# Optimization experiments

Measured on AMD Instinct MI355X. Metric: run time of the kernel, lower is better.

Reference implementation:

```python
import jax, jax.numpy as jnp
import numpy as np

B, S, T, D = 32, 8, 128, 768   # batch, num_sentences, seq_len, embedding_dim
A, L = 8, 8                    # num_args, arg_length


def _extract(sentence_embeddings, sentence_ids, token_ids):
    """Vectorized form of extract_embeddings_from_ids.

    For each (b, s, a): average, over nonzero token ids l, the embedding at the
    sentence position whose id equals token_ids[b,s,a,l]. token_id == 0 is skipped.
    sentence_ids are unique per sentence, so each id matches exactly one position
    (the only case where the original loop yields shape [B,S,A,D]).
    """
    valid = token_ids != 0                                            # [B,S,A,L]
    # match[b,s,a,l,t] = token matches sentence position t (and token is nonzero)
    match = (token_ids[..., None] == sentence_ids[:, :, None, None, :]) & valid[..., None]
    # gather matched embeddings per token: [B,S,A,L,D]
    gathered = jnp.einsum('bsalt,bstd->bsald', match.astype(sentence_embeddings.dtype),
                          sentence_embeddings)
    n_valid = jnp.maximum(valid.sum(-1), 1).astype(sentence_embeddings.dtype)  # [B,S,A]
    return gathered.sum(axis=3) / n_valid[..., None]                  # [B,S,A,D]


def setup_inputs() -> dict:
    key = jax.random.key(0)
    k_emb, k_p, k_a0, k_a1 = jax.random.split(key, 4)
    sentence_embeddings = jax.random.normal(k_emb, (B, S, T, D), dtype=jnp.float32)
    # unique token ids 1..T per sentence (0 is reserved as padding/skip)
    sentence_ids = jnp.broadcast_to(jnp.arange(1, T + 1, dtype=jnp.int64), (B, S, T))
    predicate_ids = jax.random.randint(k_p, (B, S, A, L), 0, T, dtype=jnp.int64)
    arg0_ids = jax.random.randint(k_a0, (B, S, A, L), 0, T, dtype=jnp.int64)
    arg1_ids = jax.random.randint(k_a1, (B, S, A, L), 0, T, dtype=jnp.int64)
    return {
        'sentence_embeddings': sentence_embeddings,
        'sentence_ids': sentence_ids,
        'predicate_ids': predicate_ids,
        'arg0_ids': arg0_ids,
        'arg1_ids': arg1_ids,
    }


def reference(sentence_embeddings, sentence_ids, predicate_ids, arg0_ids, arg1_ids):
    sentence_average_embeddings = sentence_embeddings.mean(axis=2)     # [B,S,D]
    predicate_embeddings = _extract(sentence_embeddings, sentence_ids, predicate_ids)
    arg0_embeddings = _extract(sentence_embeddings, sentence_ids, arg0_ids)
    arg1_embeddings = _extract(sentence_embeddings, sentence_ids, arg1_ids)
    return (sentence_average_embeddings, predicate_embeddings,
            arg0_embeddings, arg1_embeddings)
```

## Files before the change

### kernel.cpp

```cpp
#include <hip/hip_runtime.h>

namespace {
constexpr int B_ = 32, S_ = 8, T_ = 128, D_ = 768, A_ = 8, L_ = 8;
constexpr int BS = B_ * S_;
constexpr int MEAN_ELEMS = BS * D_;
constexpr int EXT_ELEMS  = BS * A_ * D_;
constexpr int TSPLIT = 4, TCH = T_ / TSPLIT;
constexpr int D4 = D_ / 4;
constexpr int RED_BLOCKS = BS * D4 / 256;
constexpr int EXT_BLOCKS = BS * A_;
constexpr size_t WS_FLOATS = (size_t)TSPLIT * BS * D_;

__global__ void __launch_bounds__(192) k_mean_partial(
    const float* __restrict__ emb, float* __restrict__ ws)
{
    int blk = blockIdx.x;
    int bs = blk >> 2, ch = blk & 3;
    int tid = threadIdx.x;
    const float4* p = reinterpret_cast<const float4*>(emb + (size_t)bs * T_ * D_)
                      + (size_t)(ch * TCH) * D4 + tid;
    float4 acc = {0.f, 0.f, 0.f, 0.f};
    #pragma unroll 8
    for (int t = 0; t < TCH; ++t) {
        float4 v = p[(size_t)t * D4];
        acc.x += v.x; acc.y += v.y; acc.z += v.z; acc.w += v.w;
    }
    reinterpret_cast<float4*>(ws)[(size_t)(ch * BS + bs) * D4 + tid] = acc;
}

__global__ void __launch_bounds__(192) k_mean_full(
    const float* __restrict__ emb, float* __restrict__ out)
{
    int bs = blockIdx.x, tid = threadIdx.x;
    const float4* p = reinterpret_cast<const float4*>(emb + (size_t)bs * T_ * D_) + tid;
    float4 acc = {0.f, 0.f, 0.f, 0.f};
    #pragma unroll 8
    for (int t = 0; t < T_; ++t) {
        float4 v = p[(size_t)t * D4];
        acc.x += v.x; acc.y += v.y; acc.z += v.z; acc.w += v.w;
    }
    const float s = 1.0f / T_;
    float4 r = {acc.x * s, acc.y * s, acc.z * s, acc.w * s};
    reinterpret_cast<float4*>(out)[(size_t)bs * D4 + tid] = r;
}

template <bool WITH_RED>
__global__ void __launch_bounds__(256) k_tail(
    const float* __restrict__ emb,
    const int* __restrict__ sids,
    const int* __restrict__ pred,
    const int* __restrict__ arg0,
    const int* __restrict__ arg1,
    const float* __restrict__ ws,
    float* __restrict__ out)
{
    int blk = blockIdx.x;
    int tid = threadIdx.x;

    if (WITH_RED) {
        if (blk < RED_BLOCKS) {
            int idx = blk * 256 + tid;
            const float4* w = reinterpret_cast<const float4*>(ws);
            float4 a = w[idx];
            float4 b = w[(size_t)BS * D4 + idx];
            float4 c = w[2 * (size_t)BS * D4 + idx];
            float4 d = w[3 * (size_t)BS * D4 + idx];
            const float s = 1.0f / T_;
            float4 r = {(a.x + b.x + c.x + d.x) * s, (a.y + b.y + c.y + d.y) * s,
                        (a.z + b.z + c.z + d.z) * s, (a.w + b.w + c.w + d.w) * s};
            reinterpret_cast<float4*>(out)[idx] = r;
            return;
        }
        blk -= RED_BLOCKS;
    }

    int bs = blk >> 3, a = blk & 7;
    constexpr int NT = 3 * L_;
    __shared__ int toks[NT];
    __shared__ int pos[NT];
    __shared__ float invs[3];

    if (tid < NT) {
        int e = tid >> 3, l = tid & 7;
        const int* p = (e == 0) ? pred : ((e == 1) ? arg0 : arg1);
        toks[tid] = p[(size_t)(bs * A_ + a) * L_ + l];
        pos[tid] = -1;
    }
    __syncthreads();
    if (tid < T_) {
        int id = sids[(size_t)bs * T_ + tid];
        #pragma unroll
        for (int i = 0; i < NT; ++i)
            if (toks[i] != 0 && toks[i] == id) pos[i] = tid;
    } else if (tid >= 128 && tid < 128 + 3) {
        int e = tid - 128, n = 0;
        #pragma unroll
        for (int l = 0; l < L_; ++l) n += (toks[e * L_ + l] != 0);
        invs[e] = 1.0f / (float)(n < 1 ? 1 : n);
    }
    __syncthreads();

    const float* base = emb + (size_t)bs * T_ * D_;
    float acc[3][3] = {};
    #pragma unroll
    for (int e = 0; e < 3; ++e) {
        #pragma unroll
        for (int l = 0; l < L_; ++l) {
            int p = pos[e * L_ + l];
            if (p >= 0) {
                const float* row = base + (size_t)p * D_;
                acc[e][0] += row[tid];
                acc[e][1] += row[tid + 256];
                acc[e][2] += row[tid + 512];
            }
        }
    }
    #pragma unroll
    for (int e = 0; e < 3; ++e) {
        float iv = invs[e];
        float* o = out + MEAN_ELEMS + (size_t)e * EXT_ELEMS + (size_t)(bs * A_ + a) * D_;
        o[tid]       = acc[e][0] * iv;
        o[tid + 256] = acc[e][1] * iv;
        o[tid + 512] = acc[e][2] * iv;
    }
}
}

extern "C" void kernel_launch(void* const* d_in, const int* in_sizes, int n_in,
                              void* d_out, int out_size, void* d_ws, size_t ws_size,
                              hipStream_t stream) {
    const float* emb  = (const float*)d_in[0];
    const int*   sids = (const int*)d_in[1];
    const int*   pred = (const int*)d_in[2];
    const int*   arg0 = (const int*)d_in[3];
    const int*   arg1 = (const int*)d_in[4];
    float* out = (float*)d_out;
    float* ws  = (float*)d_ws;

    if (ws_size >= WS_FLOATS * sizeof(float)) {
        k_mean_partial<<<dim3(BS * TSPLIT), dim3(192), 0, stream>>>(emb, ws);
        k_tail<true><<<dim3(RED_BLOCKS + EXT_BLOCKS), dim3(256), 0, stream>>>(
            emb, sids, pred, arg0, arg1, ws, out);
    } else {
        k_mean_full<<<dim3(BS), dim3(192), 0, stream>>>(emb, out);
        k_tail<false><<<dim3(EXT_BLOCKS), dim3(256), 0, stream>>>(
            emb, sids, pred, arg0, arg1, ws, out);
    }
}
```

Baseline: 45.65 us.

## Fuse sentence-mean and extraction into a single kernel launch

Replaces the two-kernel path (split-T partial mean into a workspace, then a reduce+extract kernel) with one kernel. The first 256 blocks each compute a full 128-row mean directly, and the remaining blocks do the token extraction. This removes one launch and the workspace round trip. In exchange each mean block does a long serial 128-row reduction with only 192 active threads, so the mean blocks may become the critical path.

Measured after the change: 43.85 us. 1.04x faster.

```diff
diff --git a/kernel.cpp b/kernel.cpp
--- a/kernel.cpp
+++ b/kernel.cpp
@@ -5,76 +5,39 @@
 constexpr int BS = B_ * S_;
 constexpr int MEAN_ELEMS = BS * D_;
 constexpr int EXT_ELEMS  = BS * A_ * D_;
-constexpr int TSPLIT = 4, TCH = T_ / TSPLIT;
 constexpr int D4 = D_ / 4;
-constexpr int RED_BLOCKS = BS * D4 / 256;
-constexpr int EXT_BLOCKS = BS * A_;
-constexpr size_t WS_FLOATS = (size_t)TSPLIT * BS * D_;
+constexpr int MEAN_BLOCKS = BS;
+constexpr int EXT_BLOCKS  = BS * A_;
 
-__global__ void __launch_bounds__(192) k_mean_partial(
-    const float* __restrict__ emb, float* __restrict__ ws)
-{
-    int blk = blockIdx.x;
-    int bs = blk >> 2, ch = blk & 3;
-    int tid = threadIdx.x;
-    const float4* p = reinterpret_cast<const float4*>(emb + (size_t)bs * T_ * D_)
-                      + (size_t)(ch * TCH) * D4 + tid;
-    float4 acc = {0.f, 0.f, 0.f, 0.f};
-    #pragma unroll 8
-    for (int t = 0; t < TCH; ++t) {
-        float4 v = p[(size_t)t * D4];
-        acc.x += v.x; acc.y += v.y; acc.z += v.z; acc.w += v.w;
-    }
-    reinterpret_cast<float4*>(ws)[(size_t)(ch * BS + bs) * D4 + tid] = acc;
-}
-
-__global__ void __launch_bounds__(192) k_mean_full(
-    const float* __restrict__ emb, float* __restrict__ out)
-{
-    int bs = blockIdx.x, tid = threadIdx.x;
-    const float4* p = reinterpret_cast<const float4*>(emb + (size_t)bs * T_ * D_) + tid;
-    float4 acc = {0.f, 0.f, 0.f, 0.f};
-    #pragma unroll 8
-    for (int t = 0; t < T_; ++t) {
-        float4 v = p[(size_t)t * D4];
-        acc.x += v.x; acc.y += v.y; acc.z += v.z; acc.w += v.w;
-    }
-    const float s = 1.0f / T_;
-    float4 r = {acc.x * s, acc.y * s, acc.z * s, acc.w * s};
-    reinterpret_cast<float4*>(out)[(size_t)bs * D4 + tid] = r;
-}
-
-template <bool WITH_RED>
-__global__ void __launch_bounds__(256) k_tail(
+__global__ void __launch_bounds__(256) srl_one(
     const float* __restrict__ emb,
     const int* __restrict__ sids,
     const int* __restrict__ pred,
     const int* __restrict__ arg0,
     const int* __restrict__ arg1,
-    const float* __restrict__ ws,
     float* __restrict__ out)
 {
-    int blk = blockIdx.x;
-    int tid = threadIdx.x;
+    const int blk = blockIdx.x;
+    const int tid = threadIdx.x;
 
-    if (WITH_RED) {
-        if (blk < RED_BLOCKS) {
-            int idx = blk * 256 + tid;
-            const float4* w = reinterpret_cast<const float4*>(ws);
-            float4 a = w[idx];
-            float4 b = w[(size_t)BS * D4 + idx];
-            float4 c = w[2 * (size_t)BS * D4 + idx];
-            float4 d = w[3 * (size_t)BS * D4 + idx];
-            const float s = 1.0f / T_;
-            float4 r = {(a.x + b.x + c.x + d.x) * s, (a.y + b.y + c.y + d.y) * s,
-                        (a.z + b.z + c.z + d.z) * s, (a.w + b.w + c.w + d.w) * s};
-            reinterpret_cast<float4*>(out)[idx] = r;
-            return;
+    if (blk < MEAN_BLOCKS) {
+        if (tid >= 192) return;
+        const int bs = blk;
+        const float4* p = reinterpret_cast<const float4*>(emb + (size_t)bs * T_ * D_) + tid;
+        float4 acc = {0.f, 0.f, 0.f, 0.f};
+        #pragma unroll 8
+        for (int t = 0; t < T_; ++t) {
+            float4 v = p[(size_t)t * D4];
+            acc.x += v.x; acc.y += v.y; acc.z += v.z; acc.w += v.w;
         }
-        blk -= RED_BLOCKS;
+        const float s = 1.0f / T_;
+        float4 r = {acc.x * s, acc.y * s, acc.z * s, acc.w * s};
+        reinterpret_cast<float4*>(out)[(size_t)bs * D4 + tid] = r;
+        return;
     }
 
-    int bs = blk >> 3, a = blk & 7;
+    const int eblk = blk - MEAN_BLOCKS;
+    const int bs = eblk >> 3, a = eblk & 7;
     constexpr int NT = 3 * L_;
     __shared__ int toks[NT];
     __shared__ int pos[NT];
@@ -135,15 +98,7 @@
     const int*   arg0 = (const int*)d_in[3];
     const int*   arg1 = (const int*)d_in[4];
     float* out = (float*)d_out;
-    float* ws  = (float*)d_ws;
 
-    if (ws_size >= WS_FLOATS * sizeof(float)) {
-        k_mean_partial<<<dim3(BS * TSPLIT), dim3(192), 0, stream>>>(emb, ws);
-        k_tail<true><<<dim3(RED_BLOCKS + EXT_BLOCKS), dim3(256), 0, stream>>>(
-            emb, sids, pred, arg0, arg1, ws, out);
-    } else {
-        k_mean_full<<<dim3(BS), dim3(192), 0, stream>>>(emb, out);
-        k_tail<false><<<dim3(EXT_BLOCKS), dim3(256), 0, stream>>>(
-            emb, sids, pred, arg0, arg1, ws, out);
-    }
+    srl_one<<<dim3(MEAN_BLOCKS + EXT_BLOCKS), dim3(256), 0, stream>>>(
+        emb, sids, pred, arg0, arg1, out);
 }
```
